# Kernel tuning notes

Hardware: AMD Instinct MI355X
Metric: run time of the kernel (lower is better)

## Reference

```python
import jax, jax.numpy as jnp
import numpy as np

N_NODES = 50000
N_EDGES = 800000
NEG_SLOPE = 0.2


def _edge_softmax(scores, dst, n):
    # scores: [E, H]; softmax over edges grouped by destination node
    m = jax.ops.segment_max(scores, dst, num_segments=n)          # [N, H]
    ex = jnp.exp(scores - m[dst])                                 # [E, H]
    s = jax.ops.segment_sum(ex, dst, num_segments=n)              # [N, H]
    return ex / s[dst]


def _gat_layer(h, W, attn_l, attn_r, bias, src, dst, n, heads, out_d):
    feat = (h @ W).reshape(n, heads, out_d)                       # [N, H, D]
    el = jnp.sum(feat * attn_l, axis=-1)                          # [N, H]
    er = jnp.sum(feat * attn_r, axis=-1)                          # [N, H]
    e = jax.nn.leaky_relu(el[src] + er[dst], NEG_SLOPE)           # [E, H]
    alpha = _edge_softmax(e, dst, n)                              # [E, H]
    msg = feat[src] * alpha[:, :, None]                           # [E, H, D]
    rst = jax.ops.segment_sum(msg, dst, num_segments=n)           # [N, H, D]
    return rst + bias.reshape(1, heads, out_d)


def setup_inputs() -> dict:
    key = jax.random.key(0)
    ks = jax.random.split(key, 12)
    in_dim, hid, heads, out_dim = 128, 64, 4, 64
    sc = 0.1
    return {
        "emb": jax.random.normal(ks[0], (N_NODES, in_dim), jnp.float32),
        "src": jax.random.randint(ks[1], (N_EDGES,), 0, N_NODES, jnp.int32),
        "dst": jax.random.randint(ks[2], (N_EDGES,), 0, N_NODES, jnp.int32),
        "W1": jax.random.normal(ks[3], (in_dim, heads * hid), jnp.float32) * sc,
        "attn_l1": jax.random.normal(ks[4], (1, heads, hid), jnp.float32) * sc,
        "attn_r1": jax.random.normal(ks[5], (1, heads, hid), jnp.float32) * sc,
        "b1": jax.random.normal(ks[6], (heads * hid,), jnp.float32) * sc,
        "W2": jax.random.normal(ks[7], (heads * hid, out_dim), jnp.float32) * sc,
        "attn_l2": jax.random.normal(ks[8], (1, 1, out_dim), jnp.float32) * sc,
        "attn_r2": jax.random.normal(ks[9], (1, 1, out_dim), jnp.float32) * sc,
        "b2": jax.random.normal(ks[10], (out_dim,), jnp.float32) * sc,
    }


def reference(emb, src, dst, W1, attn_l1, attn_r1, b1, W2, attn_l2, attn_r2, b2):
    n = emb.shape[0]
    h = _gat_layer(emb, W1, attn_l1, attn_r1, b1, src, dst, n, 4, 64)   # [N,4,64]
    h = jax.nn.relu(h).reshape(n, 4 * 64)                                # [N,256]
    h = _gat_layer(h, W2, attn_l2, attn_r2, b2, src, dst, n, 1, 64)      # [N,1,64]
    return h.reshape(n, 64)
```

## Files before the change

kernel.cpp:

```cpp
#include <hip/hip_runtime.h>
#include <hip/hip_bf16.h>
#include <math.h>

#define DIV_UP(a,b) (((a)+(b)-1)/(b))

typedef __attribute__((ext_vector_type(8))) short short8v;
typedef __attribute__((ext_vector_type(4))) float f32x4;

__device__ __forceinline__ float bf_lo(unsigned u){ union{unsigned x; float f;} v; v.x = u << 16; return v.f; }
__device__ __forceinline__ float bf_hi(unsigned u){ union{unsigned x; float f;} v; v.x = u & 0xffff0000u; return v.f; }
__device__ __forceinline__ unsigned short f2bf(float f){
  union{float f; unsigned u;} v; v.f = f;
  unsigned r = v.u + 0x7fff + ((v.u >> 16) & 1);
  return (unsigned short)(r >> 16);
}
__device__ __forceinline__ unsigned packbf(float a, float b){
  return (unsigned)f2bf(a) | ((unsigned)f2bf(b) << 16);
}

__global__ void k_count_deg(const int* __restrict__ dst, int* __restrict__ deg, int E){
  int i = blockIdx.x*blockDim.x + threadIdx.x;
  if (i < E) atomicAdd(&deg[dst[i]], 1);
}

__global__ __launch_bounds__(256) void k_scan1(const int* __restrict__ deg,
                                               int* __restrict__ blocksum, int N){
  int b = blockIdx.x;
  int base = b*1024 + threadIdx.x*4;
  int s = 0;
  if (base + 3 < N){
    int4 v = *(const int4*)&deg[base];
    s = v.x + v.y + v.z + v.w;
  } else {
    for (int i = 0; i < 4; i++){ int idx = base + i; if (idx < N) s += deg[idx]; }
  }
  #pragma unroll
  for (int o = 32; o; o >>= 1) s += __shfl_down(s, o);
  __shared__ int ws[4];
  int wid = threadIdx.x >> 6, lane = threadIdx.x & 63;
  if (lane == 0) ws[wid] = s;
  __syncthreads();
  if (threadIdx.x == 0) blocksum[b] = ws[0] + ws[1] + ws[2] + ws[3];
}

__global__ void k_scan2(int* __restrict__ blocksum, int nb){
  int lane = threadIdx.x;
  int carry = 0;
  for (int base = 0; base < nb; base += 64){
    int idx = base + lane;
    int orig = (idx < nb) ? blocksum[idx] : 0;
    int v = orig;
    #pragma unroll
    for (int o = 1; o < 64; o <<= 1){ int t = __shfl_up(v, o); if (lane >= o) v += t; }
    if (idx < nb) blocksum[idx] = carry + v - orig;
    carry += __shfl(v, 63);
  }
}

__global__ __launch_bounds__(256) void k_scan3(const int* __restrict__ deg,
                                               const int* __restrict__ blockoff,
                                               int* __restrict__ row_start,
                                               int* __restrict__ cursor, int N){
  int b = blockIdx.x;
  int base = b*1024 + threadIdx.x*4;
  int v[4];
  #pragma unroll
  for (int i = 0; i < 4; i++){ int idx = base + i; v[i] = (idx < N) ? deg[idx] : 0; }
  int s = v[0] + v[1] + v[2] + v[3];
  int lane = threadIdx.x & 63, wid = threadIdx.x >> 6;
  int inc = s;
  #pragma unroll
  for (int o = 1; o < 64; o <<= 1){ int t = __shfl_up(inc, o); if (lane >= o) inc += t; }
  __shared__ int wsum[4];
  if (lane == 63) wsum[wid] = inc;
  __syncthreads();
  int woff = 0;
  #pragma unroll
  for (int i = 0; i < 4; i++) if (i < wid) woff += wsum[i];
  int run = blockoff[b] + woff + inc - s;
  #pragma unroll
  for (int i = 0; i < 4; i++){
    int idx = base + i;
    if (idx < N){ row_start[idx] = run; cursor[idx] = run; run += v[i]; }
  }
  if (base < N && base + 4 >= N) row_start[N] = run;
}

__global__ void k_fill(const int* __restrict__ dst, const int* __restrict__ src,
                       int* __restrict__ cursor, int* __restrict__ srcp, int E){
  int i = blockIdx.x*blockDim.x + threadIdx.x;
  if (i < E){ int p = atomicAdd(&cursor[dst[i]], 1); srcp[p] = src[i]; }
}

template<int K, int H, bool ABF>
__global__ __launch_bounds__(256) void k_gemm_mfma(const void* __restrict__ Av,
      const float* __restrict__ B, int ldb,
      unsigned short* __restrict__ Cbf,
      const float* __restrict__ al, const float* __restrict__ ar,
      float* __restrict__ el, float* __restrict__ er, int M){
  constexpr int KP = K + 8;
  __shared__ alignas(16) __hip_bfloat16 At[64][KP];
  __shared__ alignas(16) __hip_bfloat16 Bt[64][KP];
  __shared__ float elp[2][64], erp[2][64];
  const int tid = threadIdx.x;
  const int lane = tid & 63, w = tid >> 6;
  const int mw = w >> 1, nw = w & 1;
  const int m0 = blockIdx.x * 64, by = blockIdx.y, n0 = by * 64;

  if constexpr (!ABF){
    const float* A = (const float*)Av;
    #pragma unroll
    for (int i = 0; i < K/16; i++){
      int q = tid + i*256;
      int row = q / (K/4), c4 = q % (K/4);
      float4 a = make_float4(0.f,0.f,0.f,0.f);
      if (m0 + row < M) a = *(const float4*)&A[(size_t)(m0+row)*K + c4*4];
      *(uint2*)&At[row][c4*4] = make_uint2(packbf(a.x,a.y), packbf(a.z,a.w));
    }
  } else {
    const __hip_bfloat16* A = (const __hip_bfloat16*)Av;
    #pragma unroll
    for (int i = 0; i < K/32; i++){
      int q = tid + i*256;
      int row = q / (K/8), c8 = q % (K/8);
      uint4 u = make_uint4(0,0,0,0);
      if (m0 + row < M) u = *(const uint4*)&A[(size_t)(m0+row)*K + c8*8];
      *(uint4*)&At[row][c8*8] = u;
    }
  }
  #pragma unroll
  for (int i = 0; i < K/16; i++){
    int q = tid + i*256;
    int c = q & 63, k4 = q >> 6;
    float b0 = B[(size_t)(k4*4+0)*ldb + n0 + c];
    float b1 = B[(size_t)(k4*4+1)*ldb + n0 + c];
    float b2 = B[(size_t)(k4*4+2)*ldb + n0 + c];
    float b3 = B[(size_t)(k4*4+3)*ldb + n0 + c];
    *(uint2*)&Bt[c][k4*4] = make_uint2(packbf(b0,b1), packbf(b2,b3));
  }
  __syncthreads();

  f32x4 acc[2][2];
  #pragma unroll
  for (int i = 0; i < 2; i++)
    #pragma unroll
    for (int j = 0; j < 2; j++)
      #pragma unroll
      for (int r = 0; r < 4; r++) acc[i][j][r] = 0.f;

  const int rbase = mw*32, cbase = nw*32;
  const int fr = lane & 15, fg = lane >> 4;
  #pragma unroll
  for (int ks = 0; ks < K/32; ks++){
    short8v a0 = *(const short8v*)&At[rbase + fr     ][ks*32 + fg*8];
    short8v a1 = *(const short8v*)&At[rbase + 16 + fr][ks*32 + fg*8];
    short8v b0 = *(const short8v*)&Bt[cbase + fr     ][ks*32 + fg*8];
    short8v b1 = *(const short8v*)&Bt[cbase + 16 + fr][ks*32 + fg*8];
    acc[0][0] = __builtin_amdgcn_mfma_f32_16x16x32_bf16(a0, b0, acc[0][0], 0,0,0);
    acc[0][1] = __builtin_amdgcn_mfma_f32_16x16x32_bf16(a0, b1, acc[0][1], 0,0,0);
    acc[1][0] = __builtin_amdgcn_mfma_f32_16x16x32_bf16(a1, b0, acc[1][0], 0,0,0);
    acc[1][1] = __builtin_amdgcn_mfma_f32_16x16x32_bf16(a1, b1, acc[1][1], 0,0,0);
  }

  float alv[2], arv[2];
  #pragma unroll
  for (int nt = 0; nt < 2; nt++){
    int col = cbase + nt*16 + fr;
    alv[nt] = al[by*64 + col];
    arv[nt] = ar[by*64 + col];
  }
  #pragma unroll
  for (int mt = 0; mt < 2; mt++){
    #pragma unroll
    for (int r = 0; r < 4; r++){
      float pl = acc[mt][0][r]*alv[0] + acc[mt][1][r]*alv[1];
      float pr = acc[mt][0][r]*arv[0] + acc[mt][1][r]*arv[1];
      #pragma unroll
      for (int o = 1; o < 16; o <<= 1){ pl += __shfl_xor(pl, o); pr += __shfl_xor(pr, o); }
      if (fr == 0){
        int rl = rbase + mt*16 + fg*4 + r;
        elp[nw][rl] = pl; erp[nw][rl] = pr;
      }
    }
  }
  const int NN = H*64;
  #pragma unroll
  for (int mt = 0; mt < 2; mt++){
    #pragma unroll
    for (int r = 0; r < 4; r++){
      int row = m0 + rbase + mt*16 + fg*4 + r;
      if (row < M){
        #pragma unroll
        for (int nt = 0; nt < 2; nt++)
          Cbf[(size_t)row*NN + n0 + cbase + nt*16 + fr] = f2bf(acc[mt][nt][r]);
      }
    }
  }
  __syncthreads();
  if (tid < 64){
    int row = m0 + tid;
    if (row < M){
      el[(size_t)row*H + by] = elp[0][tid] + elp[1][tid];
      er[(size_t)row*H + by] = erp[0][tid] + erp[1][tid];
    }
  }
}

__global__ __launch_bounds__(256) void k_agg4(const char* __restrict__ featb,
      const float4* __restrict__ el4, const float4* __restrict__ er4,
      const int* __restrict__ row_start, const int* __restrict__ srcp,
      const float* __restrict__ bias, __hip_bfloat16* __restrict__ outb, int N){
  __shared__ int   lds_s[4][64];
  __shared__ float lds_w[4][64*5];
  int wv = threadIdx.x >> 6, lane = threadIdx.x & 63;
  int n = blockIdx.x*4 + wv;
  if (n >= N) return;
  int g = lane >> 4, j = lane & 15, h = j >> 2;
  int rs = row_start[n], re = row_start[n+1];
  int deg = re - rs;

  float4 ern = er4[n];
  float acc[16];
  #pragma unroll
  for (int k = 0; k < 16; k++) acc[k] = 0.f;
  float S0, S1, S2, S3;

  if (deg <= 64){
    int s = 0;
    float x0 = -INFINITY, x1 = -INFINITY, x2 = -INFINITY, x3 = -INFINITY;
    if (lane < deg){
      s = srcp[rs + lane];
      float4 e4 = el4[s];
      x0 = e4.x + ern.x; x0 = x0 > 0.f ? x0 : 0.2f*x0;
      x1 = e4.y + ern.y; x1 = x1 > 0.f ? x1 : 0.2f*x1;
      x2 = e4.z + ern.z; x2 = x2 > 0.f ? x2 : 0.2f*x2;
      x3 = e4.w + ern.w; x3 = x3 > 0.f ? x3 : 0.2f*x3;
    }
    float c0 = x0, c1 = x1, c2 = x2, c3 = x3;
    #pragma unroll
    for (int o = 1; o < 64; o <<= 1){
      c0 = fmaxf(c0, __shfl_xor(c0, o)); c1 = fmaxf(c1, __shfl_xor(c1, o));
      c2 = fmaxf(c2, __shfl_xor(c2, o)); c3 = fmaxf(c3, __shfl_xor(c3, o));
    }
    float w0 = (lane < deg) ? __expf(x0 - c0) : 0.f;
    float w1 = (lane < deg) ? __expf(x1 - c1) : 0.f;
    float w2 = (lane < deg) ? __expf(x2 - c2) : 0.f;
    float w3 = (lane < deg) ? __expf(x3 - c3) : 0.f;
    float t0 = w0, t1 = w1, t2 = w2, t3 = w3;
    #pragma unroll
    for (int o = 1; o < 64; o <<= 1){
      t0 += __shfl_xor(t0, o); t1 += __shfl_xor(t1, o);
      t2 += __shfl_xor(t2, o); t3 += __shfl_xor(t3, o);
    }
    S0 = t0; S1 = t1; S2 = t2; S3 = t3;
    lds_s[wv][lane] = s;
    lds_w[wv][lane*5+0] = w0; lds_w[wv][lane*5+1] = w1;
    lds_w[wv][lane*5+2] = w2; lds_w[wv][lane*5+3] = w3;
    int iters = (deg + 3) >> 2;
    unsigned jo = (unsigned)(j << 5);
    for (int i = 0; i < iters; i += 2){
      int e0 = i*4 + g;
      int sb0 = lds_s[wv][e0];
      float wb0 = lds_w[wv][e0*5 + h];
      unsigned off0 = (unsigned)sb0*512u + jo;
      uint4 u0 = *(const uint4*)(featb + off0);
      uint4 u1 = *(const uint4*)(featb + off0 + 16);
      bool has2 = (i + 1) < iters;
      int e1 = e0 + 4;
      int sb1 = has2 ? lds_s[wv][e1] : 0;
      float wb1 = has2 ? lds_w[wv][e1*5 + h] : 0.f;
      unsigned off1 = (unsigned)sb1*512u + jo;
      uint4 v0 = *(const uint4*)(featb + off1);
      uint4 v1 = *(const uint4*)(featb + off1 + 16);
      acc[0]  += bf_lo(u0.x)*wb0; acc[1]  += bf_hi(u0.x)*wb0;
      acc[2]  += bf_lo(u0.y)*wb0; acc[3]  += bf_hi(u0.y)*wb0;
      acc[4]  += bf_lo(u0.z)*wb0; acc[5]  += bf_hi(u0.z)*wb0;
      acc[6]  += bf_lo(u0.w)*wb0; acc[7]  += bf_hi(u0.w)*wb0;
      acc[8]  += bf_lo(u1.x)*wb0; acc[9]  += bf_hi(u1.x)*wb0;
      acc[10] += bf_lo(u1.y)*wb0; acc[11] += bf_hi(u1.y)*wb0;
      acc[12] += bf_lo(u1.z)*wb0; acc[13] += bf_hi(u1.z)*wb0;
      acc[14] += bf_lo(u1.w)*wb0; acc[15] += bf_hi(u1.w)*wb0;
      acc[0]  += bf_lo(v0.x)*wb1; acc[1]  += bf_hi(v0.x)*wb1;
      acc[2]  += bf_lo(v0.y)*wb1; acc[3]  += bf_hi(v0.y)*wb1;
      acc[4]  += bf_lo(v0.z)*wb1; acc[5]  += bf_hi(v0.z)*wb1;
      acc[6]  += bf_lo(v0.w)*wb1; acc[7]  += bf_hi(v0.w)*wb1;
      acc[8]  += bf_lo(v1.x)*wb1; acc[9]  += bf_hi(v1.x)*wb1;
      acc[10] += bf_lo(v1.y)*wb1; acc[11] += bf_hi(v1.y)*wb1;
      acc[12] += bf_lo(v1.z)*wb1; acc[13] += bf_hi(v1.z)*wb1;
      acc[14] += bf_lo(v1.w)*wb1; acc[15] += bf_hi(v1.w)*wb1;
    }
  } else {
    float m0 = -INFINITY, m1 = -INFINITY, m2 = -INFINITY, m3 = -INFINITY;
    S0 = 0.f; S1 = 0.f; S2 = 0.f; S3 = 0.f;
    for (int base = rs; base < re; base += 64){
      int cnt = min(64, re - base);
      int s = 0;
      float x0 = -INFINITY, x1 = -INFINITY, x2 = -INFINITY, x3 = -INFINITY;
      if (lane < cnt){
        s = srcp[base + lane];
        float4 e4 = el4[s];
        x0 = e4.x + ern.x; x0 = x0 > 0.f ? x0 : 0.2f*x0;
        x1 = e4.y + ern.y; x1 = x1 > 0.f ? x1 : 0.2f*x1;
        x2 = e4.z + ern.z; x2 = x2 > 0.f ? x2 : 0.2f*x2;
        x3 = e4.w + ern.w; x3 = x3 > 0.f ? x3 : 0.2f*x3;
      }
      float c0 = x0, c1 = x1, c2 = x2, c3 = x3;
      #pragma unroll
      for (int o = 1; o < 64; o <<= 1){
        c0 = fmaxf(c0, __shfl_xor(c0, o)); c1 = fmaxf(c1, __shfl_xor(c1, o));
        c2 = fmaxf(c2, __shfl_xor(c2, o)); c3 = fmaxf(c3, __shfl_xor(c3, o));
      }
      float mn0 = fmaxf(m0, c0), mn1 = fmaxf(m1, c1), mn2 = fmaxf(m2, c2), mn3 = fmaxf(m3, c3);
      float sc0 = __expf(m0 - mn0), sc1 = __expf(m1 - mn1);
      float sc2 = __expf(m2 - mn2), sc3 = __expf(m3 - mn3);
      float w0 = (lane < cnt) ? __expf(x0 - mn0) : 0.f;
      float w1 = (lane < cnt) ? __expf(x1 - mn1) : 0.f;
      float w2 = (lane < cnt) ? __expf(x2 - mn2) : 0.f;
      float w3 = (lane < cnt) ? __expf(x3 - mn3) : 0.f;
      float t0 = w0, t1 = w1, t2 = w2, t3 = w3;
      #pragma unroll
      for (int o = 1; o < 64; o <<= 1){
        t0 += __shfl_xor(t0, o); t1 += __shfl_xor(t1, o);
        t2 += __shfl_xor(t2, o); t3 += __shfl_xor(t3, o);
      }
      S0 = S0*sc0 + t0; S1 = S1*sc1 + t1; S2 = S2*sc2 + t2; S3 = S3*sc3 + t3;
      m0 = mn0; m1 = mn1; m2 = mn2; m3 = mn3;
      float sch = (h == 0) ? sc0 : (h == 1) ? sc1 : (h == 2) ? sc2 : sc3;
      #pragma unroll
      for (int k = 0; k < 16; k++) acc[k] *= sch;
      lds_s[wv][lane] = s;
      lds_w[wv][lane*5+0] = w0; lds_w[wv][lane*5+1] = w1;
      lds_w[wv][lane*5+2] = w2; lds_w[wv][lane*5+3] = w3;
      int iters = (cnt + 3) >> 2;
      for (int i = 0; i < iters; i++){
        int e = i*4 + g;
        int sb  = lds_s[wv][e];
        float wb = lds_w[wv][e*5 + h];
        unsigned off = (unsigned)sb*512u + (unsigned)(j << 5);
        uint4 u0 = *(const uint4*)(featb + off);
        uint4 u1 = *(const uint4*)(featb + off + 16);
        acc[0]  += bf_lo(u0.x)*wb; acc[1]  += bf_hi(u0.x)*wb;
        acc[2]  += bf_lo(u0.y)*wb; acc[3]  += bf_hi(u0.y)*wb;
        acc[4]  += bf_lo(u0.z)*wb; acc[5]  += bf_hi(u0.z)*wb;
        acc[6]  += bf_lo(u0.w)*wb; acc[7]  += bf_hi(u0.w)*wb;
        acc[8]  += bf_lo(u1.x)*wb; acc[9]  += bf_hi(u1.x)*wb;
        acc[10] += bf_lo(u1.y)*wb; acc[11] += bf_hi(u1.y)*wb;
        acc[12] += bf_lo(u1.z)*wb; acc[13] += bf_hi(u1.z)*wb;
        acc[14] += bf_lo(u1.w)*wb; acc[15] += bf_hi(u1.w)*wb;
      }
    }
  }

  #pragma unroll
  for (int k = 0; k < 16; k++){
    acc[k] += __shfl_xor(acc[k], 16);
    acc[k] += __shfl_xor(acc[k], 32);
  }
  if (g == 0){
    float Sh = (h == 0) ? S0 : (h == 1) ? S1 : (h == 2) ? S2 : S3;
    float inv = (deg > 0) ? 1.f / Sh : 0.f;
    float4 b0 = *(const float4*)&bias[j*16 + 0];
    float4 b1 = *(const float4*)&bias[j*16 + 4];
    float4 b2 = *(const float4*)&bias[j*16 + 8];
    float4 b3 = *(const float4*)&bias[j*16 + 12];
    float v[16];
    v[0]=acc[0]*inv+b0.x;  v[1]=acc[1]*inv+b0.y;  v[2]=acc[2]*inv+b0.z;  v[3]=acc[3]*inv+b0.w;
    v[4]=acc[4]*inv+b1.x;  v[5]=acc[5]*inv+b1.y;  v[6]=acc[6]*inv+b1.z;  v[7]=acc[7]*inv+b1.w;
    v[8]=acc[8]*inv+b2.x;  v[9]=acc[9]*inv+b2.y;  v[10]=acc[10]*inv+b2.z; v[11]=acc[11]*inv+b2.w;
    v[12]=acc[12]*inv+b3.x; v[13]=acc[13]*inv+b3.y; v[14]=acc[14]*inv+b3.z; v[15]=acc[15]*inv+b3.w;
    #pragma unroll
    for (int k = 0; k < 16; k++) v[k] = fmaxf(v[k], 0.f);
    uint4 o0, o1;
    o0.x = packbf(v[0], v[1]);   o0.y = packbf(v[2], v[3]);
    o0.z = packbf(v[4], v[5]);   o0.w = packbf(v[6], v[7]);
    o1.x = packbf(v[8], v[9]);   o1.y = packbf(v[10], v[11]);
    o1.z = packbf(v[12], v[13]); o1.w = packbf(v[14], v[15]);
    uint4* op = (uint4*)outb + (size_t)n*32 + (j << 1);
    op[0] = o0; op[1] = o1;
  }
}

__global__ __launch_bounds__(256) void k_agg1(const char* __restrict__ featb,
      const float* __restrict__ el, const float* __restrict__ er,
      const int* __restrict__ row_start, const int* __restrict__ srcp,
      const float* __restrict__ bias, float* __restrict__ out, int N){
  __shared__ int   lds_s[4][64];
  __shared__ float lds_w[4][64];
  int wv = threadIdx.x >> 6, lane = threadIdx.x & 63;
  int n = blockIdx.x*4 + wv;
  if (n >= N) return;
  int g = lane >> 4, j = lane & 15;
  int rs = row_start[n], re = row_start[n+1];
  int deg = re - rs;

  float ern = er[n];
  float acc[4] = {0.f, 0.f, 0.f, 0.f};
  float S;

  if (deg <= 64){
    int s = 0;
    float x = -INFINITY;
    if (lane < deg){
      s = srcp[rs + lane];
      x = el[s] + ern;
      x = x > 0.f ? x : 0.2f*x;
    }
    float c = x;
    #pragma unroll
    for (int o = 1; o < 64; o <<= 1) c = fmaxf(c, __shfl_xor(c, o));
    float w = (lane < deg) ? __expf(x - c) : 0.f;
    float t = w;
    #pragma unroll
    for (int o = 1; o < 64; o <<= 1) t += __shfl_xor(t, o);
    S = t;
    lds_s[wv][lane] = s;
    lds_w[wv][lane] = w;
    int iters = (deg + 3) >> 2;
    unsigned jo = (unsigned)(j << 3);
    for (int i = 0; i < iters; i += 2){
      int e0 = i*4 + g;
      int sb0 = lds_s[wv][e0];
      float wb0 = lds_w[wv][e0];
      uint2 u = *(const uint2*)(featb + (unsigned)sb0*128u + jo);
      bool has2 = (i + 1) < iters;
      int e1 = e0 + 4;
      int sb1 = has2 ? lds_s[wv][e1] : 0;
      float wb1 = has2 ? lds_w[wv][e1] : 0.f;
      uint2 v2 = *(const uint2*)(featb + (unsigned)sb1*128u + jo);
      acc[0] += bf_lo(u.x)*wb0; acc[1] += bf_hi(u.x)*wb0;
      acc[2] += bf_lo(u.y)*wb0; acc[3] += bf_hi(u.y)*wb0;
      acc[0] += bf_lo(v2.x)*wb1; acc[1] += bf_hi(v2.x)*wb1;
      acc[2] += bf_lo(v2.y)*wb1; acc[3] += bf_hi(v2.y)*wb1;
    }
  } else {
    float m = -INFINITY;
    S = 0.f;
    for (int base = rs; base < re; base += 64){
      int cnt = min(64, re - base);
      int s = 0;
      float x = -INFINITY;
      if (lane < cnt){
        s = srcp[base + lane];
        x = el[s] + ern;
        x = x > 0.f ? x : 0.2f*x;
      }
      float c = x;
      #pragma unroll
      for (int o = 1; o < 64; o <<= 1) c = fmaxf(c, __shfl_xor(c, o));
      float mn = fmaxf(m, c);
      float sc = __expf(m - mn);
      float w = (lane < cnt) ? __expf(x - mn) : 0.f;
      float t = w;
      #pragma unroll
      for (int o = 1; o < 64; o <<= 1) t += __shfl_xor(t, o);
      S = S*sc + t;
      m = mn;
      #pragma unroll
      for (int k = 0; k < 4; k++) acc[k] *= sc;
      lds_s[wv][lane] = s;
      lds_w[wv][lane] = w;
      int iters = (cnt + 3) >> 2;
      for (int i = 0; i < iters; i++){
        int e = i*4 + g;
        int sb  = lds_s[wv][e];
        float wb = lds_w[wv][e];
        uint2 u = *(const uint2*)(featb + (unsigned)sb*128u + (unsigned)(j << 3));
        acc[0] += bf_lo(u.x)*wb; acc[1] += bf_hi(u.x)*wb;
        acc[2] += bf_lo(u.y)*wb; acc[3] += bf_hi(u.y)*wb;
      }
    }
  }

  #pragma unroll
  for (int k = 0; k < 4; k++){
    acc[k] += __shfl_xor(acc[k], 16);
    acc[k] += __shfl_xor(acc[k], 32);
  }
  if (g == 0){
    float inv = (deg > 0) ? 1.f / S : 0.f;
    float4 b = *(const float4*)&bias[j*4];
    float4 o;
    o.x = acc[0]*inv + b.x; o.y = acc[1]*inv + b.y;
    o.z = acc[2]*inv + b.z; o.w = acc[3]*inv + b.w;
    *(float4*)&out[(size_t)n*64 + j*4] = o;
  }
}

extern "C" void kernel_launch(void* const* d_in, const int* in_sizes, int n_in,
                              void* d_out, int out_size, void* d_ws, size_t ws_size,
                              hipStream_t stream) {
  const float* emb = (const float*)d_in[0];
  const int*   src = (const int*)d_in[1];
  const int*   dst = (const int*)d_in[2];
  const float* W1  = (const float*)d_in[3];
  const float* al1 = (const float*)d_in[4];
  const float* ar1 = (const float*)d_in[5];
  const float* b1  = (const float*)d_in[6];
  const float* W2  = (const float*)d_in[7];
  const float* al2 = (const float*)d_in[8];
  const float* ar2 = (const float*)d_in[9];
  const float* b2  = (const float*)d_in[10];
  float* out = (float*)d_out;

  const int N = in_sizes[0] / 128;
  const int E = in_sizes[1];

  char* p = (char*)d_ws;
  auto alloc = [&](size_t bytes) -> void* {
    void* r = (void*)p; p += (bytes + 255) & ~(size_t)255; return r;
  };
  __hip_bfloat16* feat1b = (__hip_bfloat16*)alloc((size_t)N*256*2);
  __hip_bfloat16* h1b    = (__hip_bfloat16*)alloc((size_t)N*256*2);
  __hip_bfloat16* feat2b = (__hip_bfloat16*)alloc((size_t)N*64*2);
  float* el1             = (float*)alloc((size_t)N*4*4);
  float* er1             = (float*)alloc((size_t)N*4*4);
  float* el2             = (float*)alloc((size_t)N*4);
  float* er2             = (float*)alloc((size_t)N*4);
  int*   deg             = (int*)alloc((size_t)N*4);
  int*   row_start       = (int*)alloc((size_t)(N+1)*4);
  int*   cursor          = (int*)alloc((size_t)N*4);
  int*   blocksum        = (int*)alloc((size_t)DIV_UP(N,1024)*4);
  int*   srcp            = (int*)alloc((size_t)E*4);

  const int nb = DIV_UP(N, 1024);

  hipMemsetAsync(deg, 0, (size_t)N*4, stream);
  k_count_deg<<<DIV_UP(E,256), 256, 0, stream>>>(dst, deg, E);
  k_scan1<<<nb, 256, 0, stream>>>(deg, blocksum, N);
  k_scan2<<<1, 64, 0, stream>>>(blocksum, nb);
  k_scan3<<<nb, 256, 0, stream>>>(deg, blocksum, row_start, cursor, N);
  k_fill<<<DIV_UP(E,256), 256, 0, stream>>>(dst, src, cursor, srcp, E);

  k_gemm_mfma<128,4,false><<<dim3(DIV_UP(N,64), 4), 256, 0, stream>>>(
      emb, W1, 256, (unsigned short*)feat1b, al1, ar1, el1, er1, N);
  k_agg4<<<DIV_UP(N,4), 256, 0, stream>>>((const char*)feat1b, (const float4*)el1,
                                          (const float4*)er1, row_start, srcp, b1, h1b, N);
  k_gemm_mfma<256,1,true><<<dim3(DIV_UP(N,64), 1), 256, 0, stream>>>(
      h1b, W2, 64, (unsigned short*)feat2b, al2, ar2, el2, er2, N);
  k_agg1<<<DIV_UP(N,4), 256, 0, stream>>>((const char*)feat2b, el2, er2,
                                          row_start, srcp, b2, out, N);
}
```

Baseline: 249.7 us.

## Precompute per-edge softmax weights without max subtraction and simplify gather kernels

Computes edge attention weights exp(leaky_relu(el+er)) during the CSR fill (layer 1) and in a separate edge kernel (layer 2), storing them in CSR order along with a dst permutation array. The aggregation kernels drop the per-node max reduction, shuffles, LDS staging and online-softmax rescaling, and instead stream weights and features directly with four-way unrolled loads, normalizing by the accumulated sum. This removes max subtraction, which relies on scores staying small enough not to overflow exp, and adds extra global traffic for the weight and dstp arrays plus one more kernel launch.

```diff
diff --git a/kernel.cpp b/kernel.cpp
--- a/kernel.cpp
+++ b/kernel.cpp
@@ -17,6 +17,7 @@
 __device__ __forceinline__ unsigned packbf(float a, float b){
   return (unsigned)f2bf(a) | ((unsigned)f2bf(b) << 16);
 }
+__device__ __forceinline__ float lrelu(float x){ return x > 0.f ? x : 0.2f*x; }
 
 __global__ void k_count_deg(const int* __restrict__ dst, int* __restrict__ deg, int E){
   int i = blockIdx.x*blockDim.x + threadIdx.x;
@@ -86,10 +87,31 @@
   if (base < N && base + 4 >= N) row_start[N] = run;
 }
 
-__global__ void k_fill(const int* __restrict__ dst, const int* __restrict__ src,
-                       int* __restrict__ cursor, int* __restrict__ srcp, int E){
+__global__ void k_fillw4(const int* __restrict__ dst, const int* __restrict__ src,
+                         int* __restrict__ cursor, int* __restrict__ srcp,
+                         int* __restrict__ dstp,
+                         const float4* __restrict__ el4, const float4* __restrict__ er4,
+                         float4* __restrict__ w4, int E){
   int i = blockIdx.x*blockDim.x + threadIdx.x;
-  if (i < E){ int p = atomicAdd(&cursor[dst[i]], 1); srcp[p] = src[i]; }
+  if (i < E){
+    int d = dst[i], s = src[i];
+    int p = atomicAdd(&cursor[d], 1);
+    srcp[p] = s; dstp[p] = d;
+    float4 l = el4[s], r = er4[d];
+    float4 w;
+    w.x = __expf(lrelu(l.x + r.x));
+    w.y = __expf(lrelu(l.y + r.y));
+    w.z = __expf(lrelu(l.z + r.z));
+    w.w = __expf(lrelu(l.w + r.w));
+    w4[p] = w;
+  }
+}
+
+__global__ void k_edgew1(const int* __restrict__ srcp, const int* __restrict__ dstp,
+                         const float* __restrict__ el, const float* __restrict__ er,
+                         float* __restrict__ w1, int E){
+  int i = blockIdx.x*blockDim.x + threadIdx.x;
+  if (i < E) w1[i] = __expf(lrelu(el[srcp[i]] + er[dstp[i]]));
 }
 
 template<int K, int H, bool ABF>
@@ -206,159 +228,61 @@
   }
 }
 
-__global__ __launch_bounds__(256) void k_agg4(const char* __restrict__ featb,
-      const float4* __restrict__ el4, const float4* __restrict__ er4,
-      const int* __restrict__ row_start, const int* __restrict__ srcp,
-      const float* __restrict__ bias, __hip_bfloat16* __restrict__ outb, int N){
-  __shared__ int   lds_s[4][64];
-  __shared__ float lds_w[4][64*5];
+__global__ __launch_bounds__(256) void k_gath4(const char* __restrict__ featb,
+      const float* __restrict__ w4, const int* __restrict__ row_start,
+      const int* __restrict__ srcp, const float* __restrict__ bias,
+      __hip_bfloat16* __restrict__ outb, int N){
   int wv = threadIdx.x >> 6, lane = threadIdx.x & 63;
   int n = blockIdx.x*4 + wv;
   if (n >= N) return;
   int g = lane >> 4, j = lane & 15, h = j >> 2;
-  int rs = row_start[n], re = row_start[n+1];
-  int deg = re - rs;
-
-  float4 ern = er4[n];
+  int rs = row_start[n], deg = row_start[n+1] - rs;
+
   float acc[16];
   #pragma unroll
   for (int k = 0; k < 16; k++) acc[k] = 0.f;
-  float S0, S1, S2, S3;
-
-  if (deg <= 64){
-    int s = 0;
-    float x0 = -INFINITY, x1 = -INFINITY, x2 = -INFINITY, x3 = -INFINITY;
-    if (lane < deg){
-      s = srcp[rs + lane];
-      float4 e4 = el4[s];
-      x0 = e4.x + ern.x; x0 = x0 > 0.f ? x0 : 0.2f*x0;
-      x1 = e4.y + ern.y; x1 = x1 > 0.f ? x1 : 0.2f*x1;
-      x2 = e4.z + ern.z; x2 = x2 > 0.f ? x2 : 0.2f*x2;
-      x3 = e4.w + ern.w; x3 = x3 > 0.f ? x3 : 0.2f*x3;
-    }
-    float c0 = x0, c1 = x1, c2 = x2, c3 = x3;
-    #pragma unroll
-    for (int o = 1; o < 64; o <<= 1){
-      c0 = fmaxf(c0, __shfl_xor(c0, o)); c1 = fmaxf(c1, __shfl_xor(c1, o));
-      c2 = fmaxf(c2, __shfl_xor(c2, o)); c3 = fmaxf(c3, __shfl_xor(c3, o));
-    }
-    float w0 = (lane < deg) ? __expf(x0 - c0) : 0.f;
-    float w1 = (lane < deg) ? __expf(x1 - c1) : 0.f;
-    float w2 = (lane < deg) ? __expf(x2 - c2) : 0.f;
-    float w3 = (lane < deg) ? __expf(x3 - c3) : 0.f;
-    float t0 = w0, t1 = w1, t2 = w2, t3 = w3;
-    #pragma unroll
-    for (int o = 1; o < 64; o <<= 1){
-      t0 += __shfl_xor(t0, o); t1 += __shfl_xor(t1, o);
-      t2 += __shfl_xor(t2, o); t3 += __shfl_xor(t3, o);
-    }
-    S0 = t0; S1 = t1; S2 = t2; S3 = t3;
-    lds_s[wv][lane] = s;
-    lds_w[wv][lane*5+0] = w0; lds_w[wv][lane*5+1] = w1;
-    lds_w[wv][lane*5+2] = w2; lds_w[wv][lane*5+3] = w3;
-    int iters = (deg + 3) >> 2;
-    unsigned jo = (unsigned)(j << 5);
-    for (int i = 0; i < iters; i += 2){
-      int e0 = i*4 + g;
-      int sb0 = lds_s[wv][e0];
-      float wb0 = lds_w[wv][e0*5 + h];
-      unsigned off0 = (unsigned)sb0*512u + jo;
-      uint4 u0 = *(const uint4*)(featb + off0);
-      uint4 u1 = *(const uint4*)(featb + off0 + 16);
-      bool has2 = (i + 1) < iters;
-      int e1 = e0 + 4;
-      int sb1 = has2 ? lds_s[wv][e1] : 0;
-      float wb1 = has2 ? lds_w[wv][e1*5 + h] : 0.f;
-      unsigned off1 = (unsigned)sb1*512u + jo;
-      uint4 v0 = *(const uint4*)(featb + off1);
-      uint4 v1 = *(const uint4*)(featb + off1 + 16);
-      acc[0]  += bf_lo(u0.x)*wb0; acc[1]  += bf_hi(u0.x)*wb0;
-      acc[2]  += bf_lo(u0.y)*wb0; acc[3]  += bf_hi(u0.y)*wb0;
-      acc[4]  += bf_lo(u0.z)*wb0; acc[5]  += bf_hi(u0.z)*wb0;
-      acc[6]  += bf_lo(u0.w)*wb0; acc[7]  += bf_hi(u0.w)*wb0;
-      acc[8]  += bf_lo(u1.x)*wb0; acc[9]  += bf_hi(u1.x)*wb0;
-      acc[10] += bf_lo(u1.y)*wb0; acc[11] += bf_hi(u1.y)*wb0;
-      acc[12] += bf_lo(u1.z)*wb0; acc[13] += bf_hi(u1.z)*wb0;
-      acc[14] += bf_lo(u1.w)*wb0; acc[15] += bf_hi(u1.w)*wb0;
-      acc[0]  += bf_lo(v0.x)*wb1; acc[1]  += bf_hi(v0.x)*wb1;
-      acc[2]  += bf_lo(v0.y)*wb1; acc[3]  += bf_hi(v0.y)*wb1;
-      acc[4]  += bf_lo(v0.z)*wb1; acc[5]  += bf_hi(v0.z)*wb1;
-      acc[6]  += bf_lo(v0.w)*wb1; acc[7]  += bf_hi(v0.w)*wb1;
-      acc[8]  += bf_lo(v1.x)*wb1; acc[9]  += bf_hi(v1.x)*wb1;
-      acc[10] += bf_lo(v1.y)*wb1; acc[11] += bf_hi(v1.y)*wb1;
-      acc[12] += bf_lo(v1.z)*wb1; acc[13] += bf_hi(v1.z)*wb1;
-      acc[14] += bf_lo(v1.w)*wb1; acc[15] += bf_hi(v1.w)*wb1;
-    }
-  } else {
-    float m0 = -INFINITY, m1 = -INFINITY, m2 = -INFINITY, m3 = -INFINITY;
-    S0 = 0.f; S1 = 0.f; S2 = 0.f; S3 = 0.f;
-    for (int base = rs; base < re; base += 64){
-      int cnt = min(64, re - base);
-      int s = 0;
-      float x0 = -INFINITY, x1 = -INFINITY, x2 = -INFINITY, x3 = -INFINITY;
-      if (lane < cnt){
-        s = srcp[base + lane];
-        float4 e4 = el4[s];
-        x0 = e4.x + ern.x; x0 = x0 > 0.f ? x0 : 0.2f*x0;
-        x1 = e4.y + ern.y; x1 = x1 > 0.f ? x1 : 0.2f*x1;
-        x2 = e4.z + ern.z; x2 = x2 > 0.f ? x2 : 0.2f*x2;
-        x3 = e4.w + ern.w; x3 = x3 > 0.f ? x3 : 0.2f*x3;
+  float Sacc = 0.f;
+  unsigned jo = (unsigned)(j << 5);
+
+  int iters = (deg + 3) >> 2;
+  for (int i = 0; i < iters; i += 4){
+    float wb[4]; uint4 u0[4], u1[4];
+    #pragma unroll
+    for (int k = 0; k < 4; k++){
+      int e = (i + k)*4 + g;
+      wb[k] = 0.f;
+      u0[k] = make_uint4(0,0,0,0); u1[k] = make_uint4(0,0,0,0);
+      if (e < deg){
+        int sb = srcp[rs + e];
+        wb[k] = w4[(size_t)(rs + e)*4 + h];
+        const char* p = featb + (size_t)sb*512u + jo;
+        u0[k] = *(const uint4*)p;
+        u1[k] = *(const uint4*)(p + 16);
       }
-      float c0 = x0, c1 = x1, c2 = x2, c3 = x3;
-      #pragma unroll
-      for (int o = 1; o < 64; o <<= 1){
-        c0 = fmaxf(c0, __shfl_xor(c0, o)); c1 = fmaxf(c1, __shfl_xor(c1, o));
-        c2 = fmaxf(c2, __shfl_xor(c2, o)); c3 = fmaxf(c3, __shfl_xor(c3, o));
-      }
-      float mn0 = fmaxf(m0, c0), mn1 = fmaxf(m1, c1), mn2 = fmaxf(m2, c2), mn3 = fmaxf(m3, c3);
-      float sc0 = __expf(m0 - mn0), sc1 = __expf(m1 - mn1);
-      float sc2 = __expf(m2 - mn2), sc3 = __expf(m3 - mn3);
-      float w0 = (lane < cnt) ? __expf(x0 - mn0) : 0.f;
-      float w1 = (lane < cnt) ? __expf(x1 - mn1) : 0.f;
-      float w2 = (lane < cnt) ? __expf(x2 - mn2) : 0.f;
-      float w3 = (lane < cnt) ? __expf(x3 - mn3) : 0.f;
-      float t0 = w0, t1 = w1, t2 = w2, t3 = w3;
-      #pragma unroll
-      for (int o = 1; o < 64; o <<= 1){
-        t0 += __shfl_xor(t0, o); t1 += __shfl_xor(t1, o);
-        t2 += __shfl_xor(t2, o); t3 += __shfl_xor(t3, o);
-      }
-      S0 = S0*sc0 + t0; S1 = S1*sc1 + t1; S2 = S2*sc2 + t2; S3 = S3*sc3 + t3;
-      m0 = mn0; m1 = mn1; m2 = mn2; m3 = mn3;
-      float sch = (h == 0) ? sc0 : (h == 1) ? sc1 : (h == 2) ? sc2 : sc3;
-      #pragma unroll
-      for (int k = 0; k < 16; k++) acc[k] *= sch;
-      lds_s[wv][lane] = s;
-      lds_w[wv][lane*5+0] = w0; lds_w[wv][lane*5+1] = w1;
-      lds_w[wv][lane*5+2] = w2; lds_w[wv][lane*5+3] = w3;
-      int iters = (cnt + 3) >> 2;
-      for (int i = 0; i < iters; i++){
-        int e = i*4 + g;
-        int sb  = lds_s[wv][e];
-        float wb = lds_w[wv][e*5 + h];
-        unsigned off = (unsigned)sb*512u + (unsigned)(j << 5);
-        uint4 u0 = *(const uint4*)(featb + off);
-        uint4 u1 = *(const uint4*)(featb + off + 16);
-        acc[0]  += bf_lo(u0.x)*wb; acc[1]  += bf_hi(u0.x)*wb;
-        acc[2]  += bf_lo(u0.y)*wb; acc[3]  += bf_hi(u0.y)*wb;
-        acc[4]  += bf_lo(u0.z)*wb; acc[5]  += bf_hi(u0.z)*wb;
-        acc[6]  += bf_lo(u0.w)*wb; acc[7]  += bf_hi(u0.w)*wb;
-        acc[8]  += bf_lo(u1.x)*wb; acc[9]  += bf_hi(u1.x)*wb;
-        acc[10] += bf_lo(u1.y)*wb; acc[11] += bf_hi(u1.y)*wb;
-        acc[12] += bf_lo(u1.z)*wb; acc[13] += bf_hi(u1.z)*wb;
-        acc[14] += bf_lo(u1.w)*wb; acc[15] += bf_hi(u1.w)*wb;
-      }
-    }
-  }
-
+    }
+    #pragma unroll
+    for (int k = 0; k < 4; k++){
+      float wk = wb[k];
+      Sacc += wk;
+      acc[0]  += bf_lo(u0[k].x)*wk; acc[1]  += bf_hi(u0[k].x)*wk;
+      acc[2]  += bf_lo(u0[k].y)*wk; acc[3]  += bf_hi(u0[k].y)*wk;
+      acc[4]  += bf_lo(u0[k].z)*wk; acc[5]  += bf_hi(u0[k].z)*wk;
+      acc[6]  += bf_lo(u0[k].w)*wk; acc[7]  += bf_hi(u0[k].w)*wk;
+      acc[8]  += bf_lo(u1[k].x)*wk; acc[9]  += bf_hi(u1[k].x)*wk;
+      acc[10] += bf_lo(u1[k].y)*wk; acc[11] += bf_hi(u1[k].y)*wk;
+      acc[12] += bf_lo(u1[k].z)*wk; acc[13] += bf_hi(u1[k].z)*wk;
+      acc[14] += bf_lo(u1[k].w)*wk; acc[15] += bf_hi(u1[k].w)*wk;
+    }
+  }
   #pragma unroll
   for (int k = 0; k < 16; k++){
     acc[k] += __shfl_xor(acc[k], 16);
     acc[k] += __shfl_xor(acc[k], 32);
   }
+  Sacc += __shfl_xor(Sacc, 16);
+  Sacc += __shfl_xor(Sacc, 32);
   if (g == 0){
-    float Sh = (h == 0) ? S0 : (h == 1) ? S1 : (h == 2) ? S2 : S3;
-    float inv = (deg > 0) ? 1.f / Sh : 0.f;
+    float inv = (deg > 0 && Sacc > 0.f) ? 1.f / Sacc : 0.f;
     float4 b0 = *(const float4*)&bias[j*16 + 0];
     float4 b1 = *(const float4*)&bias[j*16 + 4];
     float4 b2 = *(const float4*)&bias[j*16 + 8];
@@ -380,104 +304,51 @@
   }
 }
 
-__global__ __launch_bounds__(256) void k_agg1(const char* __restrict__ featb,
-      const float* __restrict__ el, const float* __restrict__ er,
-      const int* __restrict__ row_start, const int* __restrict__ srcp,
-      const float* __restrict__ bias, float* __restrict__ out, int N){
-  __shared__ int   lds_s[4][64];
-  __shared__ float lds_w[4][64];
+__global__ __launch_bounds__(256) void k_gath1(const char* __restrict__ featb,
+      const float* __restrict__ w1, const int* __restrict__ row_start,
+      const int* __restrict__ srcp, const float* __restrict__ bias,
+      float* __restrict__ out, int N){
   int wv = threadIdx.x >> 6, lane = threadIdx.x & 63;
   int n = blockIdx.x*4 + wv;
   if (n >= N) return;
   int g = lane >> 4, j = lane & 15;
-  int rs = row_start[n], re = row_start[n+1];
-  int deg = re - rs;
-
-  float ern = er[n];
+  int rs = row_start[n], deg = row_start[n+1] - rs;
+
   float acc[4] = {0.f, 0.f, 0.f, 0.f};
-  float S;
-
-  if (deg <= 64){
-    int s = 0;
-    float x = -INFINITY;
-    if (lane < deg){
-      s = srcp[rs + lane];
-      x = el[s] + ern;
-      x = x > 0.f ? x : 0.2f*x;
-    }
-    float c = x;
-    #pragma unroll
-    for (int o = 1; o < 64; o <<= 1) c = fmaxf(c, __shfl_xor(c, o));
-    float w = (lane < deg) ? __expf(x - c) : 0.f;
-    float t = w;
-    #pragma unroll
-    for (int o = 1; o < 64; o <<= 1) t += __shfl_xor(t, o);
-    S = t;
-    lds_s[wv][lane] = s;
-    lds_w[wv][lane] = w;
-    int iters = (deg + 3) >> 2;
-    unsigned jo = (unsigned)(j << 3);
-    for (int i = 0; i < iters; i += 2){
-      int e0 = i*4 + g;
-      int sb0 = lds_s[wv][e0];
-      float wb0 = lds_w[wv][e0];
-      uint2 u = *(const uint2*)(featb + (unsigned)sb0*128u + jo);
-      bool has2 = (i + 1) < iters;
-      int e1 = e0 + 4;
-      int sb1 = has2 ? lds_s[wv][e1] : 0;
-      float wb1 = has2 ? lds_w[wv][e1] : 0.f;
-      uint2 v2 = *(const uint2*)(featb + (unsigned)sb1*128u + jo);
-      acc[0] += bf_lo(u.x)*wb0; acc[1] += bf_hi(u.x)*wb0;
-      acc[2] += bf_lo(u.y)*wb0; acc[3] += bf_hi(u.y)*wb0;
-      acc[0] += bf_lo(v2.x)*wb1; acc[1] += bf_hi(v2.x)*wb1;
-      acc[2] += bf_lo(v2.y)*wb1; acc[3] += bf_hi(v2.y)*wb1;
-    }
-  } else {
-    float m = -INFINITY;
-    S = 0.f;
-    for (int base = rs; base < re; base += 64){
-      int cnt = min(64, re - base);
-      int s = 0;
-      float x = -INFINITY;
-      if (lane < cnt){
-        s = srcp[base + lane];
-        x = el[s] + ern;
-        x = x > 0.f ? x : 0.2f*x;
+  float Sacc = 0.f;
+  unsigned jo = (unsigned)(j << 3);
+
+  int iters = (deg + 3) >> 2;
+  for (int i = 0; i < iters; i += 4){
+    float wb[4]; uint2 u[4];
+    #pragma unroll
+    for (int k = 0; k < 4; k++){
+      int e = (i + k)*4 + g;
+      wb[k] = 0.f;
+      u[k] = make_uint2(0,0);
+      if (e < deg){
+        int sb = srcp[rs + e];
+        wb[k] = w1[rs + e];
+        u[k] = *(const uint2*)(featb + (size_t)sb*128u + jo);
       }
-      float c = x;
-      #pragma unroll
-      for (int o = 1; o < 64; o <<= 1) c = fmaxf(c, __shfl_xor(c, o));
-      float mn = fmaxf(m, c);
-      float sc = __expf(m - mn);
-      float w = (lane < cnt) ? __expf(x - mn) : 0.f;
-      float t = w;
-      #pragma unroll
-      for (int o = 1; o < 64; o <<= 1) t += __shfl_xor(t, o);
-      S = S*sc + t;
-      m = mn;
-      #pragma unroll
-      for (int k = 0; k < 4; k++) acc[k] *= sc;
-      lds_s[wv][lane] = s;
-      lds_w[wv][lane] = w;
-      int iters = (cnt + 3) >> 2;
-      for (int i = 0; i < iters; i++){
-        int e = i*4 + g;
-        int sb  = lds_s[wv][e];
-        float wb = lds_w[wv][e];
-        uint2 u = *(const uint2*)(featb + (unsigned)sb*128u + (unsigned)(j << 3));
-        acc[0] += bf_lo(u.x)*wb; acc[1] += bf_hi(u.x)*wb;
-        acc[2] += bf_lo(u.y)*wb; acc[3] += bf_hi(u.y)*wb;
-      }
-    }
-  }
-
+    }
+    #pragma unroll
+    for (int k = 0; k < 4; k++){
+      float wk = wb[k];
+      Sacc += wk;
+      acc[0] += bf_lo(u[k].x)*wk; acc[1] += bf_hi(u[k].x)*wk;
+      acc[2] += bf_lo(u[k].y)*wk; acc[3] += bf_hi(u[k].y)*wk;
+    }
+  }
   #pragma unroll
   for (int k = 0; k < 4; k++){
     acc[k] += __shfl_xor(acc[k], 16);
     acc[k] += __shfl_xor(acc[k], 32);
   }
+  Sacc += __shfl_xor(Sacc, 16);
+  Sacc += __shfl_xor(Sacc, 32);
   if (g == 0){
-    float inv = (deg > 0) ? 1.f / S : 0.f;
+    float inv = (deg > 0 && Sacc > 0.f) ? 1.f / Sacc : 0.f;
     float4 b = *(const float4*)&bias[j*4];
     float4 o;
     o.x = acc[0]*inv + b.x; o.y = acc[1]*inv + b.y;
@@ -521,6 +392,9 @@
   int*   cursor          = (int*)alloc((size_t)N*4);
   int*   blocksum        = (int*)alloc((size_t)DIV_UP(N,1024)*4);
   int*   srcp            = (int*)alloc((size_t)E*4);
+  int*   dstp            = (int*)alloc((size_t)E*4);
+  float* w4              = (float*)alloc((size_t)E*16);
+  float* w1              = w4;
 
   const int nb = DIV_UP(N, 1024);
 
@@ -529,14 +403,16 @@
   k_scan1<<<nb, 256, 0, stream>>>(deg, blocksum, N);
   k_scan2<<<1, 64, 0, stream>>>(blocksum, nb);
   k_scan3<<<nb, 256, 0, stream>>>(deg, blocksum, row_start, cursor, N);
-  k_fill<<<DIV_UP(E,256), 256, 0, stream>>>(dst, src, cursor, srcp, E);
 
   k_gemm_mfma<128,4,false><<<dim3(DIV_UP(N,64), 4), 256, 0, stream>>>(
       emb, W1, 256, (unsigned short*)feat1b, al1, ar1, el1, er1, N);
-  k_agg4<<<DIV_UP(N,4), 256, 0, stream>>>((const char*)feat1b, (const float4*)el1,
-                                          (const float4*)er1, row_start, srcp, b1, h1b, N);
+  k_fillw4<<<DIV_UP(E,256), 256, 0, stream>>>(dst, src, cursor, srcp, dstp,
+      (const float4*)el1, (const float4*)er1, (float4*)w4, E);
+  k_gath4<<<DIV_UP(N,4), 256, 0, stream>>>((const char*)feat1b, w4, row_start,
+                                           srcp, b1, h1b, N);
   k_gemm_mfma<256,1,true><<<dim3(DIV_UP(N,64), 1), 256, 0, stream>>>(
       h1b, W2, 64, (unsigned short*)feat2b, al2, ar2, el2, er2, N);
-  k_agg1<<<DIV_UP(N,4), 256, 0, stream>>>((const char*)feat2b, el2, er2,
-                                          row_start, srcp, b2, out, N);
-}
+  k_edgew1<<<DIV_UP(E,256), 256, 0, stream>>>(srcp, dstp, el2, er2, w1, E);
+  k_gath1<<<DIV_UP(N,4), 256, 0, stream>>>((const char*)feat2b, w1, row_start,
+                                           srcp, b2, out, N);
+}
```

After: 247.5 us. About the same (-0.9%).
